# Optimization experiments

Hardware: AMD Instinct MI355X
Metric: run time of the kernel (lower is better)

## Reference

```python
import jax, jax.numpy as jnp
import numpy as np

IN_DIM, INTER_DIM, OUT_DIM = 512, 256, 512


def setup_inputs() -> dict:
    key = jax.random.key(0)
    k1, k2, k3, k4 = jax.random.split(key, 4)
    feat_map = jax.random.normal(k1, (8, IN_DIM, 64, 64), dtype=jnp.float32)
    # xavier-uniform-style init scales
    lim_p = float(np.sqrt(6.0 / (IN_DIM + INTER_DIM)))
    lim_w = float(np.sqrt(6.0 / (IN_DIM + OUT_DIM)))
    phi_w = jax.random.uniform(k2, (INTER_DIM, IN_DIM), jnp.float32, -lim_p, lim_p)
    theta_w = jax.random.uniform(k3, (INTER_DIM, IN_DIM), jnp.float32, -lim_p, lim_p)
    weight = jax.random.uniform(k4, (IN_DIM, OUT_DIM), jnp.float32, -lim_w, lim_w)
    return {"feat_map": feat_map, "phi_w": phi_w, "theta_w": theta_w, "weight": weight}


def reference(feat_map, phi_w, theta_w, weight):
    B, D, H, W = feat_map.shape
    # b c h w -> b (h w) c
    feat_vec = jnp.transpose(feat_map.reshape(B, D, H * W), (0, 2, 1))  # [B, HW, D]
    phi = jnp.einsum('bnc,ic->bni', feat_vec, phi_w)      # [B, HW, inter]
    theta = jnp.einsum('bnc,ic->bni', feat_vec, theta_w)  # [B, HW, inter]
    product = jnp.einsum('bni,bmi->bnm', phi, theta)      # [B, HW, HW]
    phi_norm = jnp.linalg.norm(phi, axis=-1, keepdims=True)      # [B, HW, 1]
    theta_norm = jnp.linalg.norm(theta, axis=-1, keepdims=True)  # [B, HW, 1]
    norms = phi_norm * jnp.transpose(theta_norm, (0, 2, 1))      # [B, HW, HW]
    sim = jax.nn.softmax(product / norms, axis=-1)
    out = jnp.einsum('bnm,bmc->bnc', sim, feat_vec)  # [B, HW, D]
    out = jnp.einsum('bnc,cd->bnd', out, weight)     # [B, HW, out_dim]
    # b (h w) d -> b d h w
    updated = jnp.transpose(out, (0, 2, 1)).reshape(B, -1, H, W)
    return jax.nn.relu(updated)
```

## Files before the change

### kernel.cpp

```cpp
#include <hip/hip_runtime.h>


typedef short s8v __attribute__((ext_vector_type(8)));
typedef float f4v __attribute__((ext_vector_type(4)));

__device__ inline ushort f2bf(float x) {
  union { float f; unsigned u; } v; v.f = x;
  unsigned u = v.u + 0x7fff + ((v.u >> 16) & 1);
  return (ushort)(u >> 16);
}

__global__ __launch_bounds__(256) void k0a(const float* __restrict__ feat,
                                           ushort* __restrict__ featT,
                                           ushort* __restrict__ featV) {
  int bid = blockIdx.x;
  int b = bid >> 9, cb = (bid >> 6) & 7, mt = bid & 63;
  int t = threadIdx.x;
  __shared__ ushort tile[64][72];

#pragma unroll
  for (int p = 0; p < 4; p++) {
    int ci = p * 16 + (t >> 4);
    int mi = (t & 15) * 4;
    float4 v = *(const float4*)&feat[((size_t)(b * 512 + cb * 64 + ci)) * 4096 + mt * 64 + mi];
    ushort4 u; u.x = f2bf(v.x); u.y = f2bf(v.y); u.z = f2bf(v.z); u.w = f2bf(v.w);
    *(ushort4*)&featV[((size_t)(b * 64 + mt) * 512 + cb * 64 + ci) * 64 + mi] = u;
    tile[ci][mi] = u.x; tile[ci][mi + 1] = u.y; tile[ci][mi + 2] = u.z; tile[ci][mi + 3] = u.w;
  }
  __syncthreads();
  int m = t >> 2, cs = (t & 3) * 16;
  ushort tmp[16];
#pragma unroll
  for (int j = 0; j < 16; j++) tmp[j] = tile[cs + j][m];
  ushort* dst = &featT[((size_t)(b * 4096 + mt * 64 + m)) * 512 + cb * 64 + cs];
  *(s8v*)dst = *(s8v*)&tmp[0];
  *(s8v*)(dst + 8) = *(s8v*)&tmp[8];
}

__global__ __launch_bounds__(256) void k0b(const float* __restrict__ pw,
                                           const float* __restrict__ tw,
                                           ushort* __restrict__ wbp,
                                           ushort* __restrict__ wbt) {
  int bid = blockIdx.x;
  const float* src = (bid < 128) ? pw : tw;
  ushort* dst = (bid < 128) ? wbp : wbt;
  int idx = ((bid & 127) * 256 + threadIdx.x) * 4;
  float4 v = *(const float4*)&src[idx];
  ushort4 u; u.x = f2bf(v.x); u.y = f2bf(v.y); u.z = f2bf(v.z); u.w = f2bf(v.w);
  *(ushort4*)&dst[idx] = u;
}

__global__ __launch_bounds__(256) void k0c(const float* __restrict__ w,
                                           ushort* __restrict__ wT) {
  int bid = blockIdx.x;
  int cb = bid >> 3, db = bid & 7;
  int t = threadIdx.x;
  __shared__ ushort tile[64][72];
#pragma unroll
  for (int p = 0; p < 4; p++) {
    int ci = p * 16 + (t >> 4);
    int di = (t & 15) * 4;
    float4 v = *(const float4*)&w[(size_t)(cb * 64 + ci) * 512 + db * 64 + di];
    tile[ci][di] = f2bf(v.x); tile[ci][di + 1] = f2bf(v.y);
    tile[ci][di + 2] = f2bf(v.z); tile[ci][di + 3] = f2bf(v.w);
  }
  __syncthreads();
  int d = t >> 2, cs = (t & 3) * 16;
  ushort tmp[16];
#pragma unroll
  for (int j = 0; j < 16; j++) tmp[j] = tile[cs + j][d];
  ushort* dst = &wT[(size_t)(db * 64 + d) * 512 + cb * 64 + cs];
  *(s8v*)dst = *(s8v*)&tmp[0];
  *(s8v*)(dst + 8) = *(s8v*)&tmp[8];
}

__global__ __launch_bounds__(512) void k1_gemm(
    const ushort* __restrict__ featT, const ushort* __restrict__ wbp,
    const ushort* __restrict__ wbt, ushort* __restrict__ phi_n,
    ushort* __restrict__ theta_n) {
  int bid = blockIdx.x;
  int b = bid & 7;
  int rest = bid >> 3;
  int half = rest & 1;
  int nt = rest >> 1;
  const ushort* wb = half ? wbt : wbp;
  ushort* dst = half ? theta_n : phi_n;
  int t = threadIdx.x;
  int lane = t & 63, w = t >> 6;
  int col = lane & 15, quad = lane >> 4;
  int n0 = nt * 128;

  const ushort* abase =
      featT + ((size_t)(b * 4096 + n0 + w * 16 + col)) * 512 + quad * 8;

  f4v acc[16];
#pragma unroll
  for (int i = 0; i < 16; i++) acc[i] = (f4v){0.f, 0.f, 0.f, 0.f};

#pragma unroll 2
  for (int kc = 0; kc < 16; kc++) {
    s8v a = *(const s8v*)(abase + kc * 32);
#pragma unroll
    for (int it = 0; it < 16; it++) {
      s8v bf = *(const s8v*)(wb + (size_t)(it * 16 + col) * 512 + kc * 32 + quad * 8);
      acc[it] = __builtin_amdgcn_mfma_f32_16x16x32_bf16(a, bf, acc[it], 0, 0, 0);
    }
  }
  float rinv[4];
#pragma unroll
  for (int reg = 0; reg < 4; reg++) {
    float ss = 0.f;
#pragma unroll
    for (int it = 0; it < 16; it++) ss += acc[it][reg] * acc[it][reg];
    ss += __shfl_xor(ss, 1); ss += __shfl_xor(ss, 2);
    ss += __shfl_xor(ss, 4); ss += __shfl_xor(ss, 8);
    rinv[reg] = rsqrtf(ss);
  }
#pragma unroll
  for (int it = 0; it < 16; it++) {
#pragma unroll
    for (int reg = 0; reg < 4; reg++) {
      dst[((size_t)(b * 4096 + n0 + w * 16 + quad * 4 + reg)) * 256 + it * 16 + col] =
          f2bf(acc[it][reg] * rinv[reg]);
    }
  }
}

__global__ __launch_bounds__(512) void k3_attn(
    const ushort* __restrict__ phi_n, const ushort* __restrict__ theta_n,
    const ushort* __restrict__ featV, ushort* __restrict__ out1) {
  int bid = blockIdx.x;
  int b = bid & 7;
  int n0 = (bid >> 3) << 6;
  int t = threadIdx.x;
  int lane = t & 63, w = t >> 6;
  int col = lane & 15, quad = lane >> 4;
  int rg = w & 3, mh = w >> 2;
  int l32 = lane & 31, h32 = lane >> 5;

  __shared__ __align__(16) ushort ks[2 * 16384];
  __shared__ __align__(16) ushort ps[4096];
  __shared__ float dred[128];

  s8v qf[8];
  {
    const ushort* qb = phi_n + ((size_t)(b * 4096 + n0 + rg * 16 + col)) * 256 + quad * 8;
#pragma unroll
    for (int f = 0; f < 8; f++) qf[f] = *(const s8v*)(qb + f * 32);
  }

  const ushort* thb = theta_n + (size_t)b * 4096 * 256;
  const ushort* vbb = featV + (size_t)b * 64 * 512 * 64 + (size_t)(w * 64) * 64;

  f4v acc[16];
#pragma unroll
  for (int i = 0; i < 16; i++) acc[i] = (f4v){0.f, 0.f, 0.f, 0.f};
  float denp[4] = {0.f, 0.f, 0.f, 0.f};

#pragma unroll
  for (int u = 0; u < 4; u++) {
    int row = w * 8 + u * 2 + h32;
    s8v val = *(const s8v*)(thb + (size_t)row * 256 + l32 * 8);
    *(s8v*)(ks + row * 256 + ((l32 ^ (row & 7)) * 8)) = val;
  }
  __syncthreads();

#pragma unroll 1
  for (int mt = 0; mt < 64; mt++) {
    const ushort* kc_ = ks + (mt & 1) * 16384;
    ushort* kn_ = ks + ((mt & 1) ^ 1) * 16384;

    s8v kreg[4];
    if (mt < 63) {
      int m1 = (mt + 1) << 6;
#pragma unroll
      for (int u = 0; u < 4; u++) {
        int row = w * 8 + u * 2 + h32;
        kreg[u] = *(const s8v*)(thb + (size_t)(m1 + row) * 256 + l32 * 8);
      }
    }
    s8v v0[4], v1[4];
    {
      const ushort* vb = vbb + (size_t)mt * 32768;
#pragma unroll
      for (int ct = 0; ct < 4; ct++) {
        const ushort* p = vb + (ct * 16 + col) * 64 + quad * 8;
        v0[ct] = *(const s8v*)p;
        v1[ct] = *(const s8v*)(p + 32);
      }
    }

    f4v sv0 = (f4v){0.f, 0.f, 0.f, 0.f};
    f4v sv1 = (f4v){0.f, 0.f, 0.f, 0.f};
    {
      int rm = mh * 32 + col;
      const ushort* kb = kc_ + rm * 256;
#pragma unroll
      for (int kk = 0; kk < 8; kk++) {
        int pos = ((kk * 4 + quad) ^ (col & 7)) * 8;
        s8v b0 = *(const s8v*)(kb + pos);
        s8v b1 = *(const s8v*)(kb + 16 * 256 + pos);
        sv0 = __builtin_amdgcn_mfma_f32_16x16x32_bf16(qf[kk], b0, sv0, 0, 0, 0);
        sv1 = __builtin_amdgcn_mfma_f32_16x16x32_bf16(qf[kk], b1, sv1, 0, 0, 0);
      }
    }
    float p0[4], p1[4];
#pragma unroll
    for (int r = 0; r < 4; r++) {
      p0[r] = __expf(sv0[r]);
      p1[r] = __expf(sv1[r]);
      denp[r] += p0[r] + p1[r];
    }

    __syncthreads();

#pragma unroll
    for (int r = 0; r < 4; r++) {
      int n = rg * 16 + quad * 4 + r;
      int j0 = mh * 4 + (col >> 3);
      ps[n * 64 + ((j0 ^ (n & 7)) * 8) + (col & 7)] = f2bf(p0[r]);
      ps[n * 64 + (((j0 + 2) ^ (n & 7)) * 8) + (col & 7)] = f2bf(p1[r]);
    }
    if (mt < 63) {
#pragma unroll
      for (int u = 0; u < 4; u++) {
        int row = w * 8 + u * 2 + h32;
        *(s8v*)(kn_ + row * 256 + ((l32 ^ (row & 7)) * 8)) = kreg[u];
      }
    }
    __syncthreads();

#pragma unroll
    for (int rs = 0; rs < 4; rs++) {
      const ushort* pb = ps + (rs * 16 + col) * 64;
      s8v pf0 = *(const s8v*)(pb + ((quad ^ (col & 7)) * 8));
      s8v pf1 = *(const s8v*)(pb + (((quad + 4) ^ (col & 7)) * 8));
#pragma unroll
      for (int ct = 0; ct < 4; ct++) {
        acc[rs * 4 + ct] =
            __builtin_amdgcn_mfma_f32_16x16x32_bf16(pf0, v0[ct], acc[rs * 4 + ct], 0, 0, 0);
        acc[rs * 4 + ct] =
            __builtin_amdgcn_mfma_f32_16x16x32_bf16(pf1, v1[ct], acc[rs * 4 + ct], 0, 0, 0);
      }
    }
  }

#pragma unroll
  for (int r = 0; r < 4; r++) {
    float d = denp[r];
    d += __shfl_xor(d, 1); d += __shfl_xor(d, 2);
    d += __shfl_xor(d, 4); d += __shfl_xor(d, 8);
    denp[r] = d;
  }
  if (col == 0) {
#pragma unroll
    for (int r = 0; r < 4; r++) dred[mh * 64 + rg * 16 + quad * 4 + r] = denp[r];
  }
  __syncthreads();
  if (t < 64) dred[t] = 1.0f / (dred[t] + dred[64 + t]);
  __syncthreads();

#pragma unroll
  for (int rs = 0; rs < 4; rs++) {
#pragma unroll
    for (int ct = 0; ct < 4; ct++) {
#pragma unroll
      for (int reg = 0; reg < 4; reg++) {
        int n = rs * 16 + quad * 4 + reg;
        out1[((size_t)(b * 4096 + n0 + n)) * 512 + w * 64 + ct * 16 + col] =
            f2bf(acc[rs * 4 + ct][reg] * dred[n]);
      }
    }
  }
}

__global__ __launch_bounds__(512) void k4_out(
    const ushort* __restrict__ out1, const ushort* __restrict__ wT,
    float* __restrict__ out) {
  int bid = blockIdx.x;
  int b = bid & 7;
  int rest = bid >> 3;
  int dt = rest & 3;
  int nt = rest >> 2;
  int t = threadIdx.x;
  int lane = t & 63, w = t >> 6;
  int col = lane & 15, quad = lane >> 4;
  int dw = w & 1, nw = w >> 1;
  int d0 = dt * 128 + dw * 64;
  int n0 = nt * 256 + nw * 64;

  f4v acc[16];
#pragma unroll
  for (int i = 0; i < 16; i++) acc[i] = (f4v){0.f, 0.f, 0.f, 0.f};

#pragma unroll 2
  for (int kc = 0; kc < 16; kc++) {
    s8v af[4], bf[4];
#pragma unroll
    for (int rs = 0; rs < 4; rs++)
      af[rs] = *(const s8v*)(wT + (size_t)(d0 + rs * 16 + col) * 512 + kc * 32 + quad * 8);
#pragma unroll
    for (int ct = 0; ct < 4; ct++)
      bf[ct] = *(const s8v*)(out1 + ((size_t)(b * 4096 + n0 + ct * 16 + col)) * 512 +
                             kc * 32 + quad * 8);
#pragma unroll
    for (int rs = 0; rs < 4; rs++)
#pragma unroll
      for (int ct = 0; ct < 4; ct++)
        acc[rs * 4 + ct] =
            __builtin_amdgcn_mfma_f32_16x16x32_bf16(af[rs], bf[ct], acc[rs * 4 + ct], 0, 0, 0);
  }
#pragma unroll
  for (int rs = 0; rs < 4; rs++) {
#pragma unroll
    for (int ct = 0; ct < 4; ct++) {
#pragma unroll
      for (int reg = 0; reg < 4; reg++) {
        int d = d0 + rs * 16 + quad * 4 + reg;
        int n = n0 + ct * 16 + col;
        out[((size_t)(b * 512 + d)) * 4096 + n] = fmaxf(acc[rs * 4 + ct][reg], 0.f);
      }
    }
  }
}

extern "C" void kernel_launch(void* const* d_in, const int* in_sizes, int n_in,
                              void* d_out, int out_size, void* d_ws, size_t ws_size,
                              hipStream_t stream) {
  const float* feat    = (const float*)d_in[0];
  const float* phi_w   = (const float*)d_in[1];
  const float* theta_w = (const float*)d_in[2];
  const float* weight  = (const float*)d_in[3];
  float* out = (float*)d_out;

  ushort* wsu = (ushort*)d_ws;
  ushort* featT   = wsu;
  ushort* featV   = wsu + 16777216;
  ushort* phi_n   = wsu + 33554432;
  ushort* theta_n = wsu + 41943040;
  ushort* wbp     = wsu + 50331648;
  ushort* wbt     = wsu + 50462720;
  ushort* weightT = wsu + 50593792;
  ushort* out1    = wsu;

  k0a<<<dim3(4096), dim3(256), 0, stream>>>(feat, featT, featV);
  k0b<<<dim3(256), dim3(256), 0, stream>>>(phi_w, theta_w, wbp, wbt);
  k0c<<<dim3(64), dim3(256), 0, stream>>>(weight, weightT);
  k1_gemm<<<dim3(512), dim3(512), 0, stream>>>(featT, wbp, wbt, phi_n, theta_n);
  k3_attn<<<dim3(512), dim3(512), 0, stream>>>(phi_n, theta_n, featV, out1);
  k4_out<<<dim3(512), dim3(512), 0, stream>>>(out1, weightT, out);
}
```

Measured before the change: 605.6 us.

## Shrink attention key tile, single-barrier double buffering, smaller GEMM blocks

The attention kernel now processes 32-key tiles over 128 iterations, with double-buffered score and key shared memory. This allows one barrier per iteration and cuts LDS use, so more blocks can be resident (launch bounds request 4). The projection and output GEMMs switch to 256-thread blocks with twice as many blocks, for better load balance. In exchange there are more loop iterations and less work per tile for latency hiding.

```diff
diff --git a/kernel.cpp b/kernel.cpp
--- a/kernel.cpp
+++ b/kernel.cpp
@@ -74,7 +74,7 @@
   *(s8v*)(dst + 8) = *(s8v*)&tmp[8];
 }
 
-__global__ __launch_bounds__(512) void k1_gemm(
+__global__ __launch_bounds__(256) void k1_gemm(
     const ushort* __restrict__ featT, const ushort* __restrict__ wbp,
     const ushort* __restrict__ wbt, ushort* __restrict__ phi_n,
     ushort* __restrict__ theta_n) {
@@ -88,7 +88,7 @@
   int t = threadIdx.x;
   int lane = t & 63, w = t >> 6;
   int col = lane & 15, quad = lane >> 4;
-  int n0 = nt * 128;
+  int n0 = nt * 64;
 
   const ushort* abase =
       featT + ((size_t)(b * 4096 + n0 + w * 16 + col)) * 512 + quad * 8;
@@ -126,7 +126,7 @@
   }
 }
 
-__global__ __launch_bounds__(512) void k3_attn(
+__global__ __launch_bounds__(512, 4) void k3_attn(
     const ushort* __restrict__ phi_n, const ushort* __restrict__ theta_n,
     const ushort* __restrict__ featV, ushort* __restrict__ out1) {
   int bid = blockIdx.x;
@@ -136,11 +136,10 @@
   int lane = t & 63, w = t >> 6;
   int col = lane & 15, quad = lane >> 4;
   int rg = w & 3, mh = w >> 2;
-  int l32 = lane & 31, h32 = lane >> 5;
-
-  __shared__ __align__(16) ushort ks[2 * 16384];
-  __shared__ __align__(16) ushort ps[4096];
-  __shared__ float dred[128];
+
+  __shared__ __align__(16) ushort ks[2][32 * 256];
+  __shared__ __align__(16) ushort ps[2][64 * 40];
+  __shared__ float dred[2][64];
 
   s8v qf[8];
   {
@@ -150,98 +149,76 @@
   }
 
   const ushort* thb = theta_n + (size_t)b * 4096 * 256;
-  const ushort* vbb = featV + (size_t)b * 64 * 512 * 64 + (size_t)(w * 64) * 64;
+  const ushort* vbb = featV + (size_t)b * 64 * 512 * 64;
 
   f4v acc[16];
 #pragma unroll
   for (int i = 0; i < 16; i++) acc[i] = (f4v){0.f, 0.f, 0.f, 0.f};
   float denp[4] = {0.f, 0.f, 0.f, 0.f};
 
-#pragma unroll
-  for (int u = 0; u < 4; u++) {
-    int row = w * 8 + u * 2 + h32;
-    s8v val = *(const s8v*)(thb + (size_t)row * 256 + l32 * 8);
-    *(s8v*)(ks + row * 256 + ((l32 ^ (row & 7)) * 8)) = val;
+  int srow0 = w * 4 + (lane >> 5);
+  int schunk = lane & 31;
+
+#pragma unroll
+  for (int u = 0; u < 2; u++) {
+    int row = srow0 + u * 2;
+    int gc = schunk ^ (row & 7);
+    s8v val = *(const s8v*)(thb + (size_t)row * 256 + gc * 8);
+    *(s8v*)(&ks[0][row * 256 + schunk * 8]) = val;
   }
   __syncthreads();
 
 #pragma unroll 1
-  for (int mt = 0; mt < 64; mt++) {
-    const ushort* kc_ = ks + (mt & 1) * 16384;
-    ushort* kn_ = ks + ((mt & 1) ^ 1) * 16384;
-
-    s8v kreg[4];
-    if (mt < 63) {
-      int m1 = (mt + 1) << 6;
-#pragma unroll
-      for (int u = 0; u < 4; u++) {
-        int row = w * 8 + u * 2 + h32;
-        kreg[u] = *(const s8v*)(thb + (size_t)(m1 + row) * 256 + l32 * 8);
-      }
-    }
-    s8v v0[4], v1[4];
+  for (int it = 0; it < 128; it++) {
+    int cur = it & 1;
+    const ushort* kcur = &ks[cur][0];
+    ushort* pcur = &ps[cur][0];
+
+    s8v kreg0, kreg1;
+    if (it < 127) {
+      size_t mb = (size_t)(it + 1) * 32;
+      int r0 = srow0, r1 = srow0 + 2;
+      kreg0 = *(const s8v*)(thb + (mb + r0) * 256 + ((schunk ^ (r0 & 7)) * 8));
+      kreg1 = *(const s8v*)(thb + (mb + r1) * 256 + ((schunk ^ (r1 & 7)) * 8));
+    }
+    s8v vf[4];
     {
-      const ushort* vb = vbb + (size_t)mt * 32768;
-#pragma unroll
-      for (int ct = 0; ct < 4; ct++) {
-        const ushort* p = vb + (ct * 16 + col) * 64 + quad * 8;
-        v0[ct] = *(const s8v*)p;
-        v1[ct] = *(const s8v*)(p + 32);
-      }
-    }
-
-    f4v sv0 = (f4v){0.f, 0.f, 0.f, 0.f};
-    f4v sv1 = (f4v){0.f, 0.f, 0.f, 0.f};
+      const ushort* vb = vbb + ((size_t)(it >> 1)) * 512 * 64 + (it & 1) * 32 + quad * 8;
+#pragma unroll
+      for (int ct = 0; ct < 4; ct++)
+        vf[ct] = *(const s8v*)(vb + (size_t)(w * 64 + ct * 16 + col) * 64);
+    }
+    f4v sv = (f4v){0.f, 0.f, 0.f, 0.f};
     {
-      int rm = mh * 32 + col;
-      const ushort* kb = kc_ + rm * 256;
+      int row = mh * 16 + col;
+      const ushort* kb = kcur + row * 256;
 #pragma unroll
       for (int kk = 0; kk < 8; kk++) {
         int pos = ((kk * 4 + quad) ^ (col & 7)) * 8;
-        s8v b0 = *(const s8v*)(kb + pos);
-        s8v b1 = *(const s8v*)(kb + 16 * 256 + pos);
-        sv0 = __builtin_amdgcn_mfma_f32_16x16x32_bf16(qf[kk], b0, sv0, 0, 0, 0);
-        sv1 = __builtin_amdgcn_mfma_f32_16x16x32_bf16(qf[kk], b1, sv1, 0, 0, 0);
+        s8v bfrag = *(const s8v*)(kb + pos);
+        sv = __builtin_amdgcn_mfma_f32_16x16x32_bf16(qf[kk], bfrag, sv, 0, 0, 0);
       }
     }
-    float p0[4], p1[4];
 #pragma unroll
     for (int r = 0; r < 4; r++) {
-      p0[r] = __expf(sv0[r]);
-      p1[r] = __expf(sv1[r]);
-      denp[r] += p0[r] + p1[r];
-    }
-
+      float p = __expf(sv[r]);
+      denp[r] += p;
+      int n = rg * 16 + quad * 4 + r;
+      pcur[n * 40 + mh * 16 + col] = f2bf(p);
+    }
+    if (it < 127) {
+      ushort* kn = &ks[cur ^ 1][0];
+      *(s8v*)(kn + srow0 * 256 + schunk * 8) = kreg0;
+      *(s8v*)(kn + (srow0 + 2) * 256 + schunk * 8) = kreg1;
+    }
     __syncthreads();
-
-#pragma unroll
-    for (int r = 0; r < 4; r++) {
-      int n = rg * 16 + quad * 4 + r;
-      int j0 = mh * 4 + (col >> 3);
-      ps[n * 64 + ((j0 ^ (n & 7)) * 8) + (col & 7)] = f2bf(p0[r]);
-      ps[n * 64 + (((j0 + 2) ^ (n & 7)) * 8) + (col & 7)] = f2bf(p1[r]);
-    }
-    if (mt < 63) {
-#pragma unroll
-      for (int u = 0; u < 4; u++) {
-        int row = w * 8 + u * 2 + h32;
-        *(s8v*)(kn_ + row * 256 + ((l32 ^ (row & 7)) * 8)) = kreg[u];
-      }
-    }
-    __syncthreads();
-
 #pragma unroll
     for (int rs = 0; rs < 4; rs++) {
-      const ushort* pb = ps + (rs * 16 + col) * 64;
-      s8v pf0 = *(const s8v*)(pb + ((quad ^ (col & 7)) * 8));
-      s8v pf1 = *(const s8v*)(pb + (((quad + 4) ^ (col & 7)) * 8));
-#pragma unroll
-      for (int ct = 0; ct < 4; ct++) {
+      s8v pf = *(const s8v*)(pcur + (rs * 16 + col) * 40 + quad * 8);
+#pragma unroll
+      for (int ct = 0; ct < 4; ct++)
         acc[rs * 4 + ct] =
-            __builtin_amdgcn_mfma_f32_16x16x32_bf16(pf0, v0[ct], acc[rs * 4 + ct], 0, 0, 0);
-        acc[rs * 4 + ct] =
-            __builtin_amdgcn_mfma_f32_16x16x32_bf16(pf1, v1[ct], acc[rs * 4 + ct], 0, 0, 0);
-      }
+            __builtin_amdgcn_mfma_f32_16x16x32_bf16(pf, vf[ct], acc[rs * 4 + ct], 0, 0, 0);
     }
   }
 
@@ -254,10 +231,10 @@
   }
   if (col == 0) {
 #pragma unroll
-    for (int r = 0; r < 4; r++) dred[mh * 64 + rg * 16 + quad * 4 + r] = denp[r];
-  }
-  __syncthreads();
-  if (t < 64) dred[t] = 1.0f / (dred[t] + dred[64 + t]);
+    for (int r = 0; r < 4; r++) dred[mh][rg * 16 + quad * 4 + r] = denp[r];
+  }
+  __syncthreads();
+  if (t < 64) dred[0][t] = 1.0f / (dred[0][t] + dred[1][t]);
   __syncthreads();
 
 #pragma unroll
@@ -268,26 +245,25 @@
       for (int reg = 0; reg < 4; reg++) {
         int n = rs * 16 + quad * 4 + reg;
         out1[((size_t)(b * 4096 + n0 + n)) * 512 + w * 64 + ct * 16 + col] =
-            f2bf(acc[rs * 4 + ct][reg] * dred[n]);
+            f2bf(acc[rs * 4 + ct][reg] * dred[0][n]);
       }
     }
   }
 }
 
-__global__ __launch_bounds__(512) void k4_out(
+__global__ __launch_bounds__(256) void k4_out(
     const ushort* __restrict__ out1, const ushort* __restrict__ wT,
     float* __restrict__ out) {
   int bid = blockIdx.x;
   int b = bid & 7;
   int rest = bid >> 3;
-  int dt = rest & 3;
-  int nt = rest >> 2;
+  int dt = rest & 7;
+  int nt = rest >> 3;
   int t = threadIdx.x;
   int lane = t & 63, w = t >> 6;
   int col = lane & 15, quad = lane >> 4;
-  int dw = w & 1, nw = w >> 1;
-  int d0 = dt * 128 + dw * 64;
-  int n0 = nt * 256 + nw * 64;
+  int d0 = dt * 64;
+  int n0 = nt * 256 + w * 64;
 
   f4v acc[16];
 #pragma unroll
@@ -346,7 +322,7 @@
   k0a<<<dim3(4096), dim3(256), 0, stream>>>(feat, featT, featV);
   k0b<<<dim3(256), dim3(256), 0, stream>>>(phi_w, theta_w, wbp, wbt);
   k0c<<<dim3(64), dim3(256), 0, stream>>>(weight, weightT);
-  k1_gemm<<<dim3(512), dim3(512), 0, stream>>>(featT, wbp, wbt, phi_n, theta_n);
+  k1_gemm<<<dim3(1024), dim3(256), 0, stream>>>(featT, wbp, wbt, phi_n, theta_n);
   k3_attn<<<dim3(512), dim3(512), 0, stream>>>(phi_n, theta_n, featV, out1);
-  k4_out<<<dim3(512), dim3(512), 0, stream>>>(out1, weightT, out);
-}
+  k4_out<<<dim3(1024), dim3(256), 0, stream>>>(out1, weightT, out);
+}
```

Result: slower. 1.110 ms (+83.4%).
